# Kernel optimization log

Hardware: AMD Instinct MI355X
Metric: run time of the kernel (lower is better)

The kernel has to match this reference:

```python
import jax, jax.numpy as jnp
import numpy as np
import math

DIM = 4096
DV = 1024          # compress_dim
H = 16             # num_heads
NS = 32            # num_seeds
B, L = 8, 2048
EPS = 1e-5


def _layernorm(x, g, b):
    mu = jnp.mean(x, axis=-1, keepdims=True)
    var = jnp.mean((x - mu) ** 2, axis=-1, keepdims=True)
    return (x - mu) * jax.lax.rsqrt(var + EPS) * g + b


def setup_inputs() -> dict:
    key = jax.random.key(0)
    ks = jax.random.split(key, 12)
    def lin(k, out_d, in_d):
        scale = math.sqrt(6.0 / (in_d + out_d))  # xavier_uniform
        return jax.random.uniform(k, (out_d, in_d), jnp.float32, -scale, scale)
    return {
        "X": jax.random.normal(ks[0], (B, L, DIM), jnp.float32),
        "pad_mask": jax.random.randint(ks[1], (B, L), 0, 2, jnp.int32),
        "S": jax.random.uniform(ks[2], (1, NS, DV), jnp.float32, -0.05, 0.05),
        "Wq": lin(ks[3], DV, DV), "bq": jnp.zeros((DV,), jnp.float32),
        "Wk": lin(ks[4], DV, DIM), "bk": jnp.zeros((DV,), jnp.float32),
        "Wv": lin(ks[5], DV, DIM), "bv": jnp.zeros((DV,), jnp.float32),
        "Wo": lin(ks[6], DV, DV), "bo": jnp.zeros((DV,), jnp.float32),
        "g0": jnp.ones((DV,), jnp.float32), "beta0": jnp.zeros((DV,), jnp.float32),
        "g1": jnp.ones((DV,), jnp.float32), "beta1": jnp.zeros((DV,), jnp.float32),
    }


def reference(X, pad_mask, S, Wq, bq, Wk, bk, Wv, bv, Wo, bo, g0, beta0, g1, beta1):
    b, l, _ = X.shape
    dh = DV // H
    scale = 1.0 / math.sqrt(DV)  # NOTE: full dim_V, not per-head dim
    Q = jnp.broadcast_to(S, (b, NS, DV))              # seeds repeated per batch
    Qp = (Q @ Wq.T + bq).reshape(b, NS, H, dh)
    Kp = (X @ Wk.T + bk).reshape(b, l, H, dh)
    Vp = (X @ Wv.T + bv).reshape(b, l, H, dh)
    score = jnp.einsum('bqhd,bkhd->bhqk', Qp, Kp) * scale
    m = (pad_mask != 0)[:, None, None, :]             # [b,1,1,k]
    score = jnp.where(m, score, jnp.float32(-1e12))
    A = jax.nn.softmax(score, axis=-1) * m.astype(score.dtype)  # post-softmax renorm
    O = jnp.einsum('bhqk,bkhd->bqhd', A, Vp).reshape(b, NS, DV)
    O = Q + O
    O = _layernorm(O, g0, beta0)
    O = O + jax.nn.relu(O @ Wo.T + bo)
    O = _layernorm(O, g1, beta1)
    return O
```

## Files before the change

### kernel.cpp

```cpp
#include <hip/hip_runtime.h>

#define DIMX 4096
#define DVX  1024
#define HX   16
#define DHX  64
#define NSX  32
#define BX   8
#define LX   2048
#define EPSF 1e-5f

typedef unsigned short u16;
typedef unsigned int   u32;

using bf16x8 = __attribute__((ext_vector_type(8))) __bf16;
using f32x4  = __attribute__((ext_vector_type(4))) float;

__device__ __forceinline__ float bfu(u16 u) {
    union { u32 i; float f; } c; c.i = ((u32)u) << 16; return c.f;
}
__device__ __forceinline__ u16 f2b(float f) {
    union { float f; u32 u; } c; c.f = f;
    u32 u = c.u;
    u32 r = (u + 0x7fffu + ((u >> 16) & 1u)) >> 16;
    return (u16)r;
}

__device__ __forceinline__ void async16(const u16* g, u16* l) {
    __builtin_amdgcn_global_load_lds(
        (const __attribute__((address_space(1))) void*)g,
        (__attribute__((address_space(3))) void*)l, 16, 0, 0);
}

template<bool ISF>
__device__ __forceinline__ void ld8(const void* base, size_t idx, float o[8]) {
    if (ISF) {
        const float* f = (const float*)base + idx;
        float4 a = *(const float4*)f, b = *(const float4*)(f + 4);
        o[0]=a.x; o[1]=a.y; o[2]=a.z; o[3]=a.w;
        o[4]=b.x; o[5]=b.y; o[6]=b.z; o[7]=b.w;
    } else {
        const u16* h = (const u16*)base + idx;
        uint4 v = *(const uint4*)h;
        o[0]=bfu(v.x & 0xffff); o[1]=bfu(v.x >> 16);
        o[2]=bfu(v.y & 0xffff); o[3]=bfu(v.y >> 16);
        o[4]=bfu(v.z & 0xffff); o[5]=bfu(v.z >> 16);
        o[6]=bfu(v.w & 0xffff); o[7]=bfu(v.w >> 16);
    }
}
__device__ __forceinline__ float ld1(const void* base, size_t idx, bool isf) {
    return isf ? ((const float*)base)[idx] : bfu(((const u16*)base)[idx]);
}

__global__ __launch_bounds__(256) void detect_kernel(const u16* __restrict__ X,
                                                     int* __restrict__ flag) {
    __shared__ int cnt;
    if (threadIdx.x == 0) cnt = 0;
    __syncthreads();
    int local = 0;
    for (int i = threadIdx.x; i < 8192; i += 256) {
        u32 e = ((u32)X[i] >> 7) & 0xffu;
        if (e >= 200u) local++;
    }
    atomicAdd(&cnt, local);
    __syncthreads();
    if (threadIdx.x == 0) *flag = (cnt > 32) ? 1 : 0;
}

__global__ __launch_bounds__(256) void cvt_kernel(const int* __restrict__ flag,
                                                  const float* __restrict__ src,
                                                  u16* __restrict__ dst, int ngrp) {
    if (*flag == 0) return;
    int stride = gridDim.x * 256;
    for (int i = blockIdx.x * 256 + threadIdx.x; i < ngrp; i += stride) {
        const float4* f = (const float4*)(src + (size_t)i * 8);
        float4 a = f[0], b = f[1];
        uint4 r;
        r.x = (u32)f2b(a.x) | ((u32)f2b(a.y) << 16);
        r.y = (u32)f2b(a.z) | ((u32)f2b(a.w) << 16);
        r.z = (u32)f2b(b.x) | ((u32)f2b(b.y) << 16);
        r.w = (u32)f2b(b.z) | ((u32)f2b(b.w) << 16);
        *(uint4*)(dst + (size_t)i * 8) = r;
    }
}

__global__ __launch_bounds__(256) void qp_kernel(
        const int* __restrict__ flag, const void* __restrict__ S,
        const void* __restrict__ Wq, const void* __restrict__ bq,
        float* __restrict__ Qp) {
    int wid = blockIdx.x * 4 + (threadIdx.x >> 6);
    int lane = threadIdx.x & 63;
    int q = wid >> 10, n = wid & 1023;
    bool isf = (*flag != 0);
    float p = 0.f;
    if (isf) {
        const float* srow = (const float*)S + (size_t)q * DVX + lane * 16;
        const float* wrow = (const float*)Wq + (size_t)n * DVX + lane * 16;
#pragma unroll
        for (int e = 0; e < 16; e += 4) {
            float4 a = *(const float4*)(srow + e);
            float4 b = *(const float4*)(wrow + e);
            p += a.x * b.x + a.y * b.y + a.z * b.z + a.w * b.w;
        }
    } else {
        const u16* srow = (const u16*)S + (size_t)q * DVX + lane * 16;
        const u16* wrow = (const u16*)Wq + (size_t)n * DVX + lane * 16;
#pragma unroll
        for (int c = 0; c < 2; c++) {
            uint4 a = *(const uint4*)(srow + c * 8);
            uint4 b = *(const uint4*)(wrow + c * 8);
            p += bfu(a.x & 0xffff) * bfu(b.x & 0xffff) + bfu(a.x >> 16) * bfu(b.x >> 16)
               + bfu(a.y & 0xffff) * bfu(b.y & 0xffff) + bfu(a.y >> 16) * bfu(b.y >> 16)
               + bfu(a.z & 0xffff) * bfu(b.z & 0xffff) + bfu(a.z >> 16) * bfu(b.z >> 16)
               + bfu(a.w & 0xffff) * bfu(b.w & 0xffff) + bfu(a.w >> 16) * bfu(b.w >> 16);
        }
    }
#pragma unroll
    for (int off = 32; off > 0; off >>= 1)
        p += __shfl_xor(p, off, 64);
    if (lane == 0) Qp[wid] = p + ld1(bq, n, isf);
}

__global__ __launch_bounds__(512, 2) void kv_gemm3(
        const int* __restrict__ flag,
        const void* __restrict__ X,  const u16* __restrict__ Xb,
        const void* __restrict__ Wk, const void* __restrict__ bk,
        const void* __restrict__ Wv, const void* __restrict__ bv,
        const u16* __restrict__ Wkb, const u16* __restrict__ Wvb,
        u16* __restrict__ Kp, u16* __restrict__ Vp) {
    extern __shared__ __align__(16) u16 lds[];
    const bool isf = (*flag != 0);
    const u16* Xs = isf ? Xb : (const u16*)X;

    const int t = threadIdx.x;
    const int lane = t & 63, w = t >> 6;
    const int wm = w >> 2, wn = w & 3;
    const int quad = lane >> 4, l16 = lane & 15;
    const int l8 = l16 & 7;

    const int bid = blockIdx.x;
    const int swz = (bid & 7) * 64 + (bid >> 3);
    const int mt = swz >> 3, nt = swz & 7;
    const int m0 = mt * 256, n0 = nt * 256;

    const u16* Wb16; const void* bias; int boff;
    if (n0 < DVX) { Wb16 = (isf ? Wkb : (const u16*)Wk) + (size_t)n0 * DIMX;
                    bias = bk; boff = n0; }
    else          { Wb16 = (isf ? Wvb : (const u16*)Wv) + (size_t)(n0 - DVX) * DIMX;
                    bias = bv; boff = n0 - DVX; }

    f32x4 acc[8][4];
#pragma unroll
    for (int i = 0; i < 8; i++)
#pragma unroll
        for (int j = 0; j < 4; j++) acc[i][j] = {0.f, 0.f, 0.f, 0.f};

    {
        u16* An = lds;
        u16* Bn = lds + 32768;
#pragma unroll
        for (int i = 0; i < 4; i++) {
            int gi = i * 512 + t;
            int r = gi >> 3;
            int g = (gi & 7) ^ (r & 7);
            async16(Xs + (size_t)(m0 + r) * DIMX + g * 8, An + gi * 8);
        }
#pragma unroll
        for (int i = 0; i < 4; i++) {
            int gi = i * 512 + t;
            int r = gi >> 3;
            int g = (gi & 7) ^ (r & 7);
            async16(Wb16 + (size_t)r * DIMX + g * 8, Bn + gi * 8);
        }
        asm volatile("s_waitcnt vmcnt(0)" ::: "memory");
        __builtin_amdgcn_s_barrier();
    }

    for (int kt = 0; kt < DIMX / 64; kt++) {
        u16* Ab = lds + (kt & 1) * 16384;
        u16* Bb = lds + 32768 + (kt & 1) * 16384;
        u16* An = lds + ((kt + 1) & 1) * 16384;
        u16* Bn = lds + 32768 + ((kt + 1) & 1) * 16384;
        const int k1 = (kt + 1) * 64;
        const bool st = (kt + 1) < (DIMX / 64);

        bf16x8 bfr[4][2];
#pragma unroll
        for (int ni = 0; ni < 4; ni++)
#pragma unroll
            for (int ks = 0; ks < 2; ks++) {
                int R = wn * 64 + ni * 16 + l16;
                int cc = ((ks * 4 + quad) ^ l8);
                bfr[ni][ks] = *(const bf16x8*)&Bb[R * 64 + cc * 8];
            }
        {
            bf16x8 a[2][2];
#pragma unroll
            for (int dm = 0; dm < 2; dm++)
#pragma unroll
                for (int ks = 0; ks < 2; ks++) {
                    int R = wm * 128 + dm * 16 + l16;
                    int cc = ((ks * 4 + quad) ^ l8);
                    a[dm][ks] = *(const bf16x8*)&Ab[R * 64 + cc * 8];
                }
            if (st) {
#pragma unroll
                for (int i = 0; i < 4; i++) {
                    int gi = i * 512 + t;
                    int r = gi >> 3;
                    int g = (gi & 7) ^ (r & 7);
                    async16(Xs + (size_t)(m0 + r) * DIMX + k1 + g * 8, An + gi * 8);
                }
#pragma unroll
                for (int i = 0; i < 4; i++) {
                    int gi = i * 512 + t;
                    int r = gi >> 3;
                    int g = (gi & 7) ^ (r & 7);
                    async16(Wb16 + (size_t)r * DIMX + k1 + g * 8, Bn + gi * 8);
                }
            }
            __builtin_amdgcn_s_setprio(1);
#pragma unroll
            for (int dm = 0; dm < 2; dm++)
#pragma unroll
                for (int ni = 0; ni < 4; ni++)
#pragma unroll
                    for (int ks = 0; ks < 2; ks++)
                        acc[dm][ni] = __builtin_amdgcn_mfma_f32_16x16x32_bf16(
                            a[dm][ks], bfr[ni][ks], acc[dm][ni], 0, 0, 0);
            __builtin_amdgcn_s_setprio(0);
        }
        __builtin_amdgcn_s_barrier();

#pragma unroll
        for (int p = 1; p < 4; p++) {
            bf16x8 a[2][2];
#pragma unroll
            for (int dm = 0; dm < 2; dm++)
#pragma unroll
                for (int ks = 0; ks < 2; ks++) {
                    int R = wm * 128 + (2 * p + dm) * 16 + l16;
                    int cc = ((ks * 4 + quad) ^ l8);
                    a[dm][ks] = *(const bf16x8*)&Ab[R * 64 + cc * 8];
                }
            __builtin_amdgcn_s_setprio(1);
#pragma unroll
            for (int dm = 0; dm < 2; dm++)
#pragma unroll
                for (int ni = 0; ni < 4; ni++)
#pragma unroll
                    for (int ks = 0; ks < 2; ks++)
                        acc[2 * p + dm][ni] = __builtin_amdgcn_mfma_f32_16x16x32_bf16(
                            a[dm][ks], bfr[ni][ks], acc[2 * p + dm][ni], 0, 0, 0);
            __builtin_amdgcn_s_setprio(0);
            if (p < 3) __builtin_amdgcn_s_barrier();
        }

        __builtin_amdgcn_sched_barrier(0);
        asm volatile("s_waitcnt vmcnt(0)" ::: "memory");
        __builtin_amdgcn_s_barrier();
        __builtin_amdgcn_sched_barrier(0);
    }

    float bb[4];
#pragma unroll
    for (int ni = 0; ni < 4; ni++)
        bb[ni] = ld1(bias, (size_t)(boff + wn * 64 + ni * 16 + l16), isf);
#pragma unroll
    for (int mi = 0; mi < 8; mi++) {
#pragma unroll
        for (int ni = 0; ni < 4; ni++) {
            int colL = wn * 64 + ni * 16 + l16;
            int col = n0 + colL;
            u16* dst; int dcol;
            if (col < DVX) { dst = Kp; dcol = col; }
            else           { dst = Vp; dcol = col - DVX; }
#pragma unroll
            for (int r = 0; r < 4; r++) {
                int row = m0 + wm * 128 + mi * 16 + quad * 4 + r;
                dst[(size_t)row * DVX + dcol] = f2b(acc[mi][ni][r] + bb[ni]);
            }
        }
    }
}

#define TM 128
#define TN 128
#define BKK 32
#define LDT 32

__device__ __forceinline__ uint4 pack8(float o[8]) {
    uint4 r;
    r.x = (u32)f2b(o[0]) | ((u32)f2b(o[1]) << 16);
    r.y = (u32)f2b(o[2]) | ((u32)f2b(o[3]) << 16);
    r.z = (u32)f2b(o[4]) | ((u32)f2b(o[5]) << 16);
    r.w = (u32)f2b(o[6]) | ((u32)f2b(o[7]) << 16);
    return r;
}

__global__ __launch_bounds__(256) void kv_gemm2(
        const int* __restrict__ flag,
        const void* __restrict__ X,  const u16* __restrict__ Xb,
        const void* __restrict__ Wk, const void* __restrict__ bk,
        const void* __restrict__ Wv, const void* __restrict__ bv,
        const u16* __restrict__ Wkb, const u16* __restrict__ Wvb,
        u16* __restrict__ Kp, u16* __restrict__ Vp) {
    __shared__ u16 As[TM * LDT];
    __shared__ u16 Bs[TN * LDT];
    const bool isf = (*flag != 0);
    const u16* Xs = isf ? Xb : (const u16*)X;

    const int t = threadIdx.x;
    const int lane = t & 63, w = t >> 6;
    const int wm = w >> 1, wn = w & 1;
    const int quad = lane >> 4, l16 = lane & 15;
    const int bl = blockIdx.x;
    const int xcd = bl & 7, bq = bl >> 3;
    const int m0 = (xcd + 8 * (bq >> 4)) * TM;
    const int n0 = (bq & 15) * TN;
    const u16* Wb16; const void* bias; int boff;
    if (n0 < DVX) { Wb16 = (isf ? Wkb : (const u16*)Wk) + (size_t)n0 * DIMX;
                    bias = bk; boff = n0; }
    else          { Wb16 = (isf ? Wvb : (const u16*)Wv) + (size_t)(n0 - DVX) * DIMX;
                    bias = bv; boff = n0 - DVX; }

    f32x4 acc[4][4];
#pragma unroll
    for (int i = 0; i < 4; i++)
#pragma unroll
        for (int j = 0; j < 4; j++) acc[i][j] = {0.f, 0.f, 0.f, 0.f};

    const int srow = lane >> 2;
    const int gcol = ((lane & 3) ^ ((lane >> 3) & 3)) * 8;
    const int ph = (l16 >> 1) & 3;

    for (int k0 = 0; k0 < DIMX; k0 += BKK) {
        __syncthreads();
#pragma unroll
        for (int c = 0; c < 2; c++) {
            int rr = w * 32 + c * 16;
            async16(Xs + (size_t)(m0 + rr + srow) * DIMX + k0 + gcol,
                    As + rr * LDT);
            async16(Wb16 + (size_t)(rr + srow) * DIMX + k0 + gcol,
                    Bs + rr * LDT);
        }
        __syncthreads();
        bf16x8 af[4], bfr[4];
#pragma unroll
        for (int mi = 0; mi < 4; mi++) {
            int ar = wm * 64 + mi * 16 + l16;
            af[mi] = *(const bf16x8*)&As[ar * LDT + (quad ^ ph) * 8];
        }
#pragma unroll
        for (int ni = 0; ni < 4; ni++) {
            int br = wn * 64 + ni * 16 + l16;
            bfr[ni] = *(const bf16x8*)&Bs[br * LDT + (quad ^ ph) * 8];
        }
#pragma unroll
        for (int mi = 0; mi < 4; mi++)
#pragma unroll
            for (int ni = 0; ni < 4; ni++)
                acc[mi][ni] = __builtin_amdgcn_mfma_f32_16x16x32_bf16(
                    af[mi], bfr[ni], acc[mi][ni], 0, 0, 0);
    }

#pragma unroll
    for (int mi = 0; mi < 4; mi++) {
#pragma unroll
        for (int ni = 0; ni < 4; ni++) {
            int colL = wn * 64 + ni * 16 + l16;
            int col = n0 + colL;
            float bb = ld1(bias, (size_t)(boff + colL), isf);
            u16* dst; int dcol;
            if (col < DVX) { dst = Kp; dcol = col; }
            else           { dst = Vp; dcol = col - DVX; }
#pragma unroll
            for (int r = 0; r < 4; r++) {
                int row = m0 + wm * 64 + mi * 16 + quad * 4 + r;
                dst[(size_t)row * DVX + dcol] = f2b(acc[mi][ni][r] + bb);
            }
        }
    }
}

template<bool ISF>
__device__ void kv_body(const void* __restrict__ X,
                        const void* __restrict__ Wk, const void* __restrict__ bk,
                        const void* __restrict__ Wv, const void* __restrict__ bv,
                        u16* __restrict__ Kp, u16* __restrict__ Vp,
                        u16* As, u16* Bs) {
    const int t = threadIdx.x;
    const int lane = t & 63, w = t >> 6;
    const int wm = w >> 1, wn = w & 1;
    const int quad = lane >> 4, l16 = lane & 15;
    const int bl = blockIdx.x;
    const int xcd = bl & 7, bq = bl >> 3;
    const int m0 = (xcd + 8 * (bq >> 4)) * TM;
    const int n0 = (bq & 15) * TN;
    const void* Wbase; const void* bias; int boff;
    size_t woff;
    if (n0 < DVX) { Wbase = Wk; bias = bk; woff = (size_t)n0 * DIMX; boff = n0; }
    else          { Wbase = Wv; bias = bv; woff = (size_t)(n0 - DVX) * DIMX; boff = n0 - DVX; }
    const u16* Wb16 = (const u16*)Wbase + woff;
    const float* Wbf = (const float*)Wbase + woff;

    f32x4 acc[4][4];
#pragma unroll
    for (int i = 0; i < 4; i++)
#pragma unroll
        for (int j = 0; j < 4; j++) acc[i][j] = {0.f, 0.f, 0.f, 0.f};

    const int srow = lane >> 2;
    const int gcol = ((lane & 3) ^ ((lane >> 3) & 3)) * 8;
    const int ph = (l16 >> 1) & 3;
    const int r0 = t >> 2, c0 = (t & 3) * 8;
    const int r1 = r0 + 64;
    const int swc = (((t & 3) ^ ((r0 >> 1) & 3))) * 8;

    for (int k0 = 0; k0 < DIMX; k0 += BKK) {
        if constexpr (ISF) {
            float oa0[8], oa1[8], ob0[8], ob1[8];
            ld8<true>(X,   (size_t)(m0 + r0) * DIMX + k0 + c0, oa0);
            ld8<true>(X,   (size_t)(m0 + r1) * DIMX + k0 + c0, oa1);
            ld8<true>(Wbf, (size_t)r0 * DIMX + k0 + c0, ob0);
            ld8<true>(Wbf, (size_t)r1 * DIMX + k0 + c0, ob1);
            __syncthreads();
            *(uint4*)&As[r0 * LDT + swc] = pack8(oa0);
            *(uint4*)&As[r1 * LDT + swc] = pack8(oa1);
            *(uint4*)&Bs[r0 * LDT + swc] = pack8(ob0);
            *(uint4*)&Bs[r1 * LDT + swc] = pack8(ob1);
        } else {
            __syncthreads();
#pragma unroll
            for (int c = 0; c < 2; c++) {
                int rr = w * 32 + c * 16;
                async16((const u16*)X + (size_t)(m0 + rr + srow) * DIMX + k0 + gcol,
                        As + rr * LDT);
                async16(Wb16 + (size_t)(rr + srow) * DIMX + k0 + gcol,
                        Bs + rr * LDT);
            }
        }
        __syncthreads();
        bf16x8 af[4], bfr[4];
#pragma unroll
        for (int mi = 0; mi < 4; mi++) {
            int ar = wm * 64 + mi * 16 + l16;
            af[mi] = *(const bf16x8*)&As[ar * LDT + (quad ^ ph) * 8];
        }
#pragma unroll
        for (int ni = 0; ni < 4; ni++) {
            int br = wn * 64 + ni * 16 + l16;
            bfr[ni] = *(const bf16x8*)&Bs[br * LDT + (quad ^ ph) * 8];
        }
#pragma unroll
        for (int mi = 0; mi < 4; mi++)
#pragma unroll
            for (int ni = 0; ni < 4; ni++)
                acc[mi][ni] = __builtin_amdgcn_mfma_f32_16x16x32_bf16(
                    af[mi], bfr[ni], acc[mi][ni], 0, 0, 0);
    }

#pragma unroll
    for (int mi = 0; mi < 4; mi++) {
#pragma unroll
        for (int ni = 0; ni < 4; ni++) {
            int colL = wn * 64 + ni * 16 + l16;
            int col = n0 + colL;
            float bb = ld1(bias, (size_t)(boff + colL), ISF);
            u16* dst; int dcol;
            if (col < DVX) { dst = Kp; dcol = col; }
            else           { dst = Vp; dcol = col - DVX; }
#pragma unroll
            for (int r = 0; r < 4; r++) {
                int row = m0 + wm * 64 + mi * 16 + quad * 4 + r;
                dst[(size_t)row * DVX + dcol] = f2b(acc[mi][ni][r] + bb);
            }
        }
    }
}

__global__ __launch_bounds__(256) void kv_gemm(
        const int* __restrict__ flag, const void* __restrict__ X,
        const void* __restrict__ Wk, const void* __restrict__ bk,
        const void* __restrict__ Wv, const void* __restrict__ bv,
        u16* __restrict__ Kp, u16* __restrict__ Vp) {
    __shared__ u16 As[TM * LDT];
    __shared__ u16 Bs[TN * LDT];
    if (*flag) kv_body<true>(X, Wk, bk, Wv, bv, Kp, Vp, As, Bs);
    else       kv_body<false>(X, Wk, bk, Wv, bv, Kp, Vp, As, Bs);
}

#define CHK 256
#define NCH (LX / CHK)
__global__ __launch_bounds__(256) void attn2_kernel(
        const float* __restrict__ Qp, const u16* __restrict__ Kp,
        const u16* __restrict__ Vp, const int* __restrict__ pad,
        float* __restrict__ Opart, float* __restrict__ Ml) {
    __shared__ float sc[NSX * CHK];
    const int blk = blockIdx.x;
    const int b  = blk / (HX * NCH);
    const int h  = (blk / NCH) % HX;
    const int c0 = blk % NCH;
    const int t = threadIdx.x;
    const int w = t >> 6, lane = t & 63;
    const int rsub = lane >> 3;
    const int dsub = lane & 7;
    const int q0w = w * 8;

    float qc[8][8];
#pragma unroll
    for (int qq = 0; qq < 8; qq++) {
        const float* qp = Qp + (size_t)(q0w + qq) * DVX + h * DHX + dsub * 8;
        float4 a = *(const float4*)qp, bq4 = *(const float4*)(qp + 4);
        qc[qq][0]=a.x; qc[qq][1]=a.y; qc[qq][2]=a.z; qc[qq][3]=a.w;
        qc[qq][4]=bq4.x; qc[qq][5]=bq4.y; qc[qq][6]=bq4.z; qc[qq][7]=bq4.w;
    }

    const u16* kb = Kp + ((size_t)b * LX + c0 * CHK) * DVX + h * DHX;
    const int* pb = pad + b * LX + c0 * CHK;

    float lmax[8];
#pragma unroll
    for (int qq = 0; qq < 8; qq++) lmax[qq] = -3e38f;
    for (int i = 0; i < CHK / 8; i++) {
        int k = i * 8 + rsub;
        uint4 v = *(const uint4*)(kb + (size_t)k * DVX + dsub * 8);
        float kf[8];
        kf[0]=bfu(v.x & 0xffff); kf[1]=bfu(v.x >> 16);
        kf[2]=bfu(v.y & 0xffff); kf[3]=bfu(v.y >> 16);
        kf[4]=bfu(v.z & 0xffff); kf[5]=bfu(v.z >> 16);
        kf[6]=bfu(v.w & 0xffff); kf[7]=bfu(v.w >> 16);
        int pm = pb[k];
#pragma unroll
        for (int qq = 0; qq < 8; qq++) {
            float s = kf[0]*qc[qq][0] + kf[1]*qc[qq][1]
                    + kf[2]*qc[qq][2] + kf[3]*qc[qq][3]
                    + kf[4]*qc[qq][4] + kf[5]*qc[qq][5]
                    + kf[6]*qc[qq][6] + kf[7]*qc[qq][7];
            s += __shfl_xor(s, 1, 64);
            s += __shfl_xor(s, 2, 64);
            s += __shfl_xor(s, 4, 64);
            s *= 0.03125f;
            s = pm ? s : -1e30f;
            if (dsub == 0) sc[(q0w + qq) * CHK + k] = s;
            lmax[qq] = fmaxf(lmax[qq], s);
        }
    }
#pragma unroll
    for (int qq = 0; qq < 8; qq++) {
        lmax[qq] = fmaxf(lmax[qq], __shfl_xor(lmax[qq], 8, 64));
        lmax[qq] = fmaxf(lmax[qq], __shfl_xor(lmax[qq], 16, 64));
        lmax[qq] = fmaxf(lmax[qq], __shfl_xor(lmax[qq], 32, 64));
    }

#pragma unroll
    for (int qq = 0; qq < 8; qq++) {
        float m = lmax[qq];
        float lsum = 0.f;
#pragma unroll
        for (int it = 0; it < CHK / 64; it++) {
            int idx = (q0w + qq) * CHK + it * 64 + lane;
            float sv = sc[idx];
            float e = (sv > -1e29f) ? __expf(sv - m) : 0.f;
            sc[idx] = e;
            lsum += e;
        }
#pragma unroll
        for (int off = 32; off > 0; off >>= 1)
            lsum += __shfl_xor(lsum, off, 64);
        if (lane == 0) {
            Ml[(size_t)blk * 64 + (q0w + qq) * 2 + 0] = m;
            Ml[(size_t)blk * 64 + (q0w + qq) * 2 + 1] = lsum;
        }
    }

    float acc[8][8];
#pragma unroll
    for (int qq = 0; qq < 8; qq++)
#pragma unroll
        for (int e = 0; e < 8; e++) acc[qq][e] = 0.f;
    const u16* vb = Vp + ((size_t)b * LX + c0 * CHK) * DVX + h * DHX + dsub * 8;
    for (int i = 0; i < CHK / 8; i++) {
        int k = i * 8 + rsub;
        uint4 v = *(const uint4*)(vb + (size_t)k * DVX);
        float vf[8];
        vf[0]=bfu(v.x & 0xffff); vf[1]=bfu(v.x >> 16);
        vf[2]=bfu(v.y & 0xffff); vf[3]=bfu(v.y >> 16);
        vf[4]=bfu(v.z & 0xffff); vf[5]=bfu(v.z >> 16);
        vf[6]=bfu(v.w & 0xffff); vf[7]=bfu(v.w >> 16);
#pragma unroll
        for (int qq = 0; qq < 8; qq++) {
            float p = sc[(q0w + qq) * CHK + k];
#pragma unroll
            for (int e = 0; e < 8; e++) acc[qq][e] += p * vf[e];
        }
    }
#pragma unroll
    for (int qq = 0; qq < 8; qq++) {
#pragma unroll
        for (int e = 0; e < 8; e++) {
            acc[qq][e] += __shfl_xor(acc[qq][e], 8, 64);
            acc[qq][e] += __shfl_xor(acc[qq][e], 16, 64);
            acc[qq][e] += __shfl_xor(acc[qq][e], 32, 64);
        }
        if (rsub == qq) {
            float* op = Opart + ((size_t)blk * NSX + q0w + qq) * DHX + dsub * 8;
            float4 r0 = {acc[qq][0], acc[qq][1], acc[qq][2], acc[qq][3]};
            float4 r1 = {acc[qq][4], acc[qq][5], acc[qq][6], acc[qq][7]};
            *(float4*)op = r0;
            *(float4*)(op + 4) = r1;
        }
    }
}

__global__ __launch_bounds__(256) void attn_combine(
        const float* __restrict__ Opart, const float* __restrict__ Ml,
        float* __restrict__ Oat) {
    const int bh = blockIdx.x;
    const int b = bh / HX, h = bh % HX;
    const int t = threadIdx.x;
    const int q = t >> 3, d0 = (t & 7) * 8;
    const size_t cbase = (size_t)bh * NCH;
    float m = -3e38f;
#pragma unroll
    for (int c = 0; c < NCH; c++)
        m = fmaxf(m, Ml[(cbase + c) * 64 + q * 2]);
    float l = 0.f, o[8];
#pragma unroll
    for (int e = 0; e < 8; e++) o[e] = 0.f;
#pragma unroll
    for (int c = 0; c < NCH; c++) {
        float mc = Ml[(cbase + c) * 64 + q * 2 + 0];
        float lc = Ml[(cbase + c) * 64 + q * 2 + 1];
        float wgt = (mc > -1e29f) ? __expf(mc - m) : 0.f;
        l += wgt * lc;
        const float* op = Opart + ((cbase + c) * NSX + q) * DHX + d0;
        float4 x = *(const float4*)op, y = *(const float4*)(op + 4);
        o[0] += wgt * x.x; o[1] += wgt * x.y; o[2] += wgt * x.z; o[3] += wgt * x.w;
        o[4] += wgt * y.x; o[5] += wgt * y.y; o[6] += wgt * y.z; o[7] += wgt * y.w;
    }
    float inv = (l > 0.f) ? 1.f / l : 0.f;
    float* dst = Oat + ((size_t)(b * NSX) + q) * DVX + h * DHX + d0;
    float4 r0 = {o[0]*inv, o[1]*inv, o[2]*inv, o[3]*inv};
    float4 r1 = {o[4]*inv, o[5]*inv, o[6]*inv, o[7]*inv};
    *(float4*)dst = r0;
    *(float4*)(dst + 4) = r1;
}

#define QG 4
__global__ __launch_bounds__(256) void attn_kernel(
        const float* __restrict__ Qp, const u16* __restrict__ Kp,
        const u16* __restrict__ Vp, const int* __restrict__ pad,
        float* __restrict__ Oat) {
    __shared__ float qv[QG * DHX];
    __shared__ float sc[QG * LX];
    __shared__ float rpart[256 * 8];
    __shared__ float invs[QG];
    const int blk = blockIdx.x;
    const int nqg = NSX / QG;
    const int b  = blk / (HX * nqg);
    const int h  = (blk / nqg) % HX;
    const int q0 = (blk % nqg) * QG;
    const int t = threadIdx.x;
    const int w = t >> 6, lane = t & 63;

    qv[t] = Qp[(size_t)(q0 + (t >> 6)) * DVX + h * DHX + (t & 63)];
    __syncthreads();

    const u16* Kb = Kp + (size_t)b * LX * DVX + h * DHX;
    const int rsub = lane >> 3;
    const int dsub = lane & 7;
    float qc[8];
#pragma unroll
    for (int e = 0; e < 8; e++) qc[e] = qv[w * DHX + dsub * 8 + e];

    float lmax = -3e38f;
    for (int i = 0; i < LX / 8; i++) {
        int k = i * 8 + rsub;
        uint4 v = *(const uint4*)(Kb + (size_t)k * DVX + dsub * 8);
        float s = bfu(v.x & 0xffff) * qc[0] + bfu(v.x >> 16) * qc[1]
                + bfu(v.y & 0xffff) * qc[2] + bfu(v.y >> 16) * qc[3]
                + bfu(v.z & 0xffff) * qc[4] + bfu(v.z >> 16) * qc[5]
                + bfu(v.w & 0xffff) * qc[6] + bfu(v.w >> 16) * qc[7];
        s += __shfl_xor(s, 1, 64);
        s += __shfl_xor(s, 2, 64);
        s += __shfl_xor(s, 4, 64);
        s *= 0.03125f;
        s = (pad[b * LX + k] != 0) ? s : -1e30f;
        if (dsub == 0) sc[w * LX + k] = s;
        lmax = fmaxf(lmax, s);
    }
#pragma unroll
    for (int off = 32; off > 0; off >>= 1)
        lmax = fmaxf(lmax, __shfl_xor(lmax, off, 64));
    float lsum = 0.f;
    for (int i = 0; i < LX / 64; i++) {
        int k = i * 64 + lane;
        float sv = sc[w * LX + k];
        float e = (sv > -1e29f) ? __expf(sv - lmax) : 0.f;
        sc[w * LX + k] = e;
        lsum += e;
    }
#pragma unroll
    for (int off = 32; off > 0; off >>= 1)
        lsum += __shfl_xor(lsum, off, 64);
    if (lane == 0) invs[w] = (lsum > 0.f) ? 1.f / lsum : 0.f;

    const int kg = (t >> 3) & 7, dg = t & 7;
    const u16* Vb = Vp + (size_t)b * LX * DVX + h * DHX + dg * 8;
    float a8[8];
#pragma unroll
    for (int e = 0; e < 8; e++) a8[e] = 0.f;
    for (int i = 0; i < LX / 8; i++) {
        int k = i * 8 + kg;
        float p = sc[w * LX + k];
        uint4 v = *(const uint4*)(Vb + (size_t)k * DVX);
        a8[0] += p * bfu(v.x & 0xffff); a8[1] += p * bfu(v.x >> 16);
        a8[2] += p * bfu(v.y & 0xffff); a8[3] += p * bfu(v.y >> 16);
        a8[4] += p * bfu(v.z & 0xffff); a8[5] += p * bfu(v.z >> 16);
        a8[6] += p * bfu(v.w & 0xffff); a8[7] += p * bfu(v.w >> 16);
    }
#pragma unroll
    for (int e = 0; e < 8; e++) rpart[t * 8 + e] = a8[e];
    __syncthreads();

    {
        int q = t >> 6, d = t & 63;
        float o = 0.f;
#pragma unroll
        for (int g = 0; g < 8; g++)
            o += rpart[(q * 64 + g * 8 + (d >> 3)) * 8 + (d & 7)];
        o *= invs[q];
        Oat[((size_t)(b * NSX + q0 + q)) * DVX + h * DHX + d] = o;
    }
}

template<bool ISF>
__device__ void epi_body(float* u, float* y0, float* red,
                         const float* __restrict__ Oat, const void* __restrict__ S,
                         const void* __restrict__ Wo, const void* __restrict__ bo,
                         const void* __restrict__ g0, const void* __restrict__ be0,
                         const void* __restrict__ g1, const void* __restrict__ be1,
                         void* __restrict__ out) {
    const int bq = blockIdx.x;
    const int q = bq & 31;
    const int t = threadIdx.x;
    const int w = t >> 6, lane = t & 63;

    float ls = 0.f, ls2 = 0.f;
#pragma unroll
    for (int j = 0; j < 2; j++) {
        int c = t + 512 * j;
        float v = ld1(S, (size_t)q * DVX + c, ISF) + Oat[(size_t)bq * DVX + c];
        u[c] = v; ls += v; ls2 += v * v;
    }
    red[t] = ls; __syncthreads();
    for (int s2 = 256; s2 > 0; s2 >>= 1) { if (t < s2) red[t] += red[t + s2]; __syncthreads(); }
    float mu = red[0] / DVX; __syncthreads();
    red[t] = ls2; __syncthreads();
    for (int s2 = 256; s2 > 0; s2 >>= 1) { if (t < s2) red[t] += red[t + s2]; __syncthreads(); }
    float var = red[0] / DVX - mu * mu;
    float r = rsqrtf(var + EPSF);
    __syncthreads();
#pragma unroll
    for (int j = 0; j < 2; j++) {
        int c = t + 512 * j;
        y0[c] = (u[c] - mu) * r * ld1(g0, c, ISF) + ld1(be0, c, ISF);
    }
    __syncthreads();

    float yr[16];
    if constexpr (ISF) {
#pragma unroll
        for (int e = 0; e < 16; e++) yr[e] = y0[lane * 16 + e];
    } else {
#pragma unroll
        for (int e = 0; e < 8; e++) { yr[e] = y0[lane * 8 + e]; yr[8 + e] = y0[512 + lane * 8 + e]; }
    }
    for (int i = 0; i < 128; i++) {
        int n = i * 8 + w;
        float p = 0.f;
        if constexpr (ISF) {
            float wv[8];
            const float* row = (const float*)Wo + (size_t)n * DVX;
            ld8<true>(row, lane * 16, wv);
#pragma unroll
            for (int e = 0; e < 8; e++) p += wv[e] * yr[e];
            ld8<true>(row, lane * 16 + 8, wv);
#pragma unroll
            for (int e = 0; e < 8; e++) p += wv[e] * yr[8 + e];
        } else {
            const uint4* row = (const uint4*)((const u16*)Wo + (size_t)n * DVX);
            uint4 v0 = row[lane], v1 = row[lane + 64];
            p += bfu(v0.x & 0xffff) * yr[0] + bfu(v0.x >> 16) * yr[1]
               + bfu(v0.y & 0xffff) * yr[2] + bfu(v0.y >> 16) * yr[3]
               + bfu(v0.z & 0xffff) * yr[4] + bfu(v0.z >> 16) * yr[5]
               + bfu(v0.w & 0xffff) * yr[6] + bfu(v0.w >> 16) * yr[7];
            p += bfu(v1.x & 0xffff) * yr[8]  + bfu(v1.x >> 16) * yr[9]
               + bfu(v1.y & 0xffff) * yr[10] + bfu(v1.y >> 16) * yr[11]
               + bfu(v1.z & 0xffff) * yr[12] + bfu(v1.z >> 16) * yr[13]
               + bfu(v1.w & 0xffff) * yr[14] + bfu(v1.w >> 16) * yr[15];
        }
#pragma unroll
        for (int off = 32; off > 0; off >>= 1)
            p += __shfl_xor(p, off, 64);
        if (lane == 0) {
            float z = p + ld1(bo, n, ISF);
            u[n] = y0[n] + fmaxf(z, 0.f);
        }
    }
    __syncthreads();
    ls = 0.f; ls2 = 0.f;
#pragma unroll
    for (int j = 0; j < 2; j++) {
        int c = t + 512 * j; float v = u[c]; ls += v; ls2 += v * v;
    }
    red[t] = ls; __syncthreads();
    for (int s2 = 256; s2 > 0; s2 >>= 1) { if (t < s2) red[t] += red[t + s2]; __syncthreads(); }
    mu = red[0] / DVX; __syncthreads();
    red[t] = ls2; __syncthreads();
    for (int s2 = 256; s2 > 0; s2 >>= 1) { if (t < s2) red[t] += red[t + s2]; __syncthreads(); }
    var = red[0] / DVX - mu * mu;
    r = rsqrtf(var + EPSF);
#pragma unroll
    for (int j = 0; j < 2; j++) {
        int c = t + 512 * j;
        float v = (u[c] - mu) * r * ld1(g1, c, ISF) + ld1(be1, c, ISF);
        if (ISF) ((float*)out)[(size_t)bq * DVX + c] = v;
        else     ((u16*)out)[(size_t)bq * DVX + c] = f2b(v);
    }
}

__global__ __launch_bounds__(512) void epi_kernel(
        const int* __restrict__ flag,
        const float* __restrict__ Oat, const void* __restrict__ S,
        const void* __restrict__ Wo, const void* __restrict__ bo,
        const void* __restrict__ g0, const void* __restrict__ be0,
        const void* __restrict__ g1, const void* __restrict__ be1,
        void* __restrict__ out) {
    __shared__ float u[DVX];
    __shared__ float y0[DVX];
    __shared__ float red[512];
    if (*flag) epi_body<true>(u, y0, red, Oat, S, Wo, bo, g0, be0, g1, be1, out);
    else       epi_body<false>(u, y0, red, Oat, S, Wo, bo, g0, be0, g1, be1, out);
}

extern "C" void kernel_launch(void* const* d_in, const int* in_sizes, int n_in,
                              void* d_out, int out_size, void* d_ws, size_t ws_size,
                              hipStream_t stream) {
    (void)in_sizes; (void)n_in; (void)out_size;
    const void* X    = d_in[0];
    const int* pad   = (const int*)d_in[1];
    const void* S    = d_in[2];
    const void* Wq   = d_in[3];
    const void* bq   = d_in[4];
    const void* Wk   = d_in[5];
    const void* bk   = d_in[6];
    const void* Wv   = d_in[7];
    const void* bv   = d_in[8];
    const void* Wo   = d_in[9];
    const void* bo   = d_in[10];
    const void* g0   = d_in[11];
    const void* be0  = d_in[12];
    const void* g1   = d_in[13];
    const void* be1  = d_in[14];

    char* ws = (char*)d_ws;
    int*   flag = (int*)ws;
    float* Qp  = (float*)(ws + 256);
    float* Oat = (float*)(ws + 256 + 131072);
    u16*   Kp  = (u16*)(ws + 256 + 131072 + 1048576);
    u16*   Vp  = Kp + (size_t)BX * LX * DVX;
    u16*   Xb  = Vp + (size_t)BX * LX * DVX;
    u16*   Wkb = Xb + (size_t)BX * LX * DIMX;
    u16*   Wvb = Wkb + (size_t)DVX * DIMX;
    float* Opart = (float*)(Wvb + (size_t)DVX * DIMX);
    float* Ml  = Opart + (size_t)BX * HX * NCH * NSX * DHX;

    size_t need = 256 + 131072 + 1048576
                + 2 * (size_t)BX * LX * DVX * 2
                + (size_t)BX * LX * DIMX * 2
                + 2 * (size_t)DVX * DIMX * 2;
    size_t need2 = need
                 + (size_t)BX * HX * NCH * NSX * DHX * 4
                 + (size_t)BX * HX * NCH * 64 * 4;

    static int attr_ok = -1;
    if (attr_ok < 0) {
        hipError_t e = hipFuncSetAttribute(
            reinterpret_cast<const void*>(kv_gemm3),
            hipFuncAttributeMaxDynamicSharedMemorySize, 131072);
        attr_ok = (e == hipSuccess) ? 1 : 0;
    }

    detect_kernel<<<1, 256, 0, stream>>>((const u16*)X, flag);
    qp_kernel<<<8192, 256, 0, stream>>>(flag, S, Wq, bq, Qp);

    if (ws_size >= need) {
        cvt_kernel<<<2048, 256, 0, stream>>>(flag, (const float*)X, Xb,
                                             BX * LX * DIMX / 8);
        cvt_kernel<<<512, 256, 0, stream>>>(flag, (const float*)Wk, Wkb,
                                            DVX * DIMX / 8);
        cvt_kernel<<<512, 256, 0, stream>>>(flag, (const float*)Wv, Wvb,
                                            DVX * DIMX / 8);
        if (attr_ok == 1) {
            kv_gemm3<<<512, 512, 131072, stream>>>(flag, X, Xb, Wk, bk, Wv, bv,
                                                   Wkb, Wvb, Kp, Vp);
        } else {
            kv_gemm2<<<2048, 256, 0, stream>>>(flag, X, Xb, Wk, bk, Wv, bv,
                                               Wkb, Wvb, Kp, Vp);
        }
    } else {
        kv_gemm<<<2048, 256, 0, stream>>>(flag, X, Wk, bk, Wv, bv, Kp, Vp);
    }

    if (ws_size >= need2) {
        attn2_kernel<<<BX * HX * NCH, 256, 0, stream>>>(Qp, Kp, Vp, pad,
                                                        Opart, Ml);
        attn_combine<<<BX * HX, 256, 0, stream>>>(Opart, Ml, Oat);
    } else {
        attn_kernel<<<BX * HX * (NSX / QG), 256, 0, stream>>>(Qp, Kp, Vp, pad, Oat);
    }
    epi_kernel<<<BX * NSX, 512, 0, stream>>>(flag, Oat, S, Wo, bo, g0, be0, g1, be1, (void*)d_out);
}
```

Before: 887.1 us.

## Hoist async prefetch before MFMA loop and coalesce fp32 row dot products

In the K/V projection GEMM main loop, the next tile's global-to-LDS async loads are now issued at the top of each iteration, and the intermediate barriers between the four MFMA sub-phases are removed. The goal is to overlap memory traffic with the whole compute phase and cut synchronisation stalls. Separately, the fp32 Qp and Wo row dot products now read with a lane-interleaved float4 stride, so a wave's accesses are contiguous and coalesced. Issuing the prefetch earlier may raise register pressure, and fewer barriers change how waves interleave.

```diff
diff --git a/kernel.cpp b/kernel.cpp
--- a/kernel.cpp
+++ b/kernel.cpp
@@ -93,12 +93,12 @@
     bool isf = (*flag != 0);
     float p = 0.f;
     if (isf) {
-        const float* srow = (const float*)S + (size_t)q * DVX + lane * 16;
-        const float* wrow = (const float*)Wq + (size_t)n * DVX + lane * 16;
-#pragma unroll
-        for (int e = 0; e < 16; e += 4) {
-            float4 a = *(const float4*)(srow + e);
-            float4 b = *(const float4*)(wrow + e);
+        const float4* s4 = (const float4*)((const float*)S + (size_t)q * DVX);
+        const float4* w4 = (const float4*)((const float*)Wq + (size_t)n * DVX);
+#pragma unroll
+        for (int e = 0; e < 4; e++) {
+            float4 a = s4[e * 64 + lane];
+            float4 b = w4[e * 64 + lane];
             p += a.x * b.x + a.y * b.y + a.z * b.z + a.w * b.w;
         }
     } else {
@@ -181,7 +181,24 @@
         u16* An = lds + ((kt + 1) & 1) * 16384;
         u16* Bn = lds + 32768 + ((kt + 1) & 1) * 16384;
         const int k1 = (kt + 1) * 64;
-        const bool st = (kt + 1) < (DIMX / 64);
+
+        if (kt + 1 < DIMX / 64) {
+#pragma unroll
+            for (int i = 0; i < 4; i++) {
+                int gi = i * 512 + t;
+                int r = gi >> 3;
+                int g = (gi & 7) ^ (r & 7);
+                async16(Xs + (size_t)(m0 + r) * DIMX + k1 + g * 8, An + gi * 8);
+            }
+#pragma unroll
+            for (int i = 0; i < 4; i++) {
+                int gi = i * 512 + t;
+                int r = gi >> 3;
+                int g = (gi & 7) ^ (r & 7);
+                async16(Wb16 + (size_t)r * DIMX + k1 + g * 8, Bn + gi * 8);
+            }
+        }
+        __builtin_amdgcn_sched_barrier(0);
 
         bf16x8 bfr[4][2];
 #pragma unroll
@@ -192,47 +209,9 @@
                 int cc = ((ks * 4 + quad) ^ l8);
                 bfr[ni][ks] = *(const bf16x8*)&Bb[R * 64 + cc * 8];
             }
-        {
-            bf16x8 a[2][2];
-#pragma unroll
-            for (int dm = 0; dm < 2; dm++)
-#pragma unroll
-                for (int ks = 0; ks < 2; ks++) {
-                    int R = wm * 128 + dm * 16 + l16;
-                    int cc = ((ks * 4 + quad) ^ l8);
-                    a[dm][ks] = *(const bf16x8*)&Ab[R * 64 + cc * 8];
-                }
-            if (st) {
-#pragma unroll
-                for (int i = 0; i < 4; i++) {
-                    int gi = i * 512 + t;
-                    int r = gi >> 3;
-                    int g = (gi & 7) ^ (r & 7);
-                    async16(Xs + (size_t)(m0 + r) * DIMX + k1 + g * 8, An + gi * 8);
-                }
-#pragma unroll
-                for (int i = 0; i < 4; i++) {
-                    int gi = i * 512 + t;
-                    int r = gi >> 3;
-                    int g = (gi & 7) ^ (r & 7);
-                    async16(Wb16 + (size_t)r * DIMX + k1 + g * 8, Bn + gi * 8);
-                }
-            }
-            __builtin_amdgcn_s_setprio(1);
-#pragma unroll
-            for (int dm = 0; dm < 2; dm++)
-#pragma unroll
-                for (int ni = 0; ni < 4; ni++)
-#pragma unroll
-                    for (int ks = 0; ks < 2; ks++)
-                        acc[dm][ni] = __builtin_amdgcn_mfma_f32_16x16x32_bf16(
-                            a[dm][ks], bfr[ni][ks], acc[dm][ni], 0, 0, 0);
-            __builtin_amdgcn_s_setprio(0);
-        }
-        __builtin_amdgcn_s_barrier();
-
-#pragma unroll
-        for (int p = 1; p < 4; p++) {
+
+#pragma unroll
+        for (int p = 0; p < 4; p++) {
             bf16x8 a[2][2];
 #pragma unroll
             for (int dm = 0; dm < 2; dm++)
@@ -252,7 +231,6 @@
                         acc[2 * p + dm][ni] = __builtin_amdgcn_mfma_f32_16x16x32_bf16(
                             a[dm][ks], bfr[ni][ks], acc[2 * p + dm][ni], 0, 0, 0);
             __builtin_amdgcn_s_setprio(0);
-            if (p < 3) __builtin_amdgcn_s_barrier();
         }
 
         __builtin_amdgcn_sched_barrier(0);
@@ -770,8 +748,12 @@
 
     float yr[16];
     if constexpr (ISF) {
-#pragma unroll
-        for (int e = 0; e < 16; e++) yr[e] = y0[lane * 16 + e];
+        const float4* y4 = (const float4*)y0;
+#pragma unroll
+        for (int e = 0; e < 4; e++) {
+            float4 v = y4[e * 64 + lane];
+            yr[e*4+0]=v.x; yr[e*4+1]=v.y; yr[e*4+2]=v.z; yr[e*4+3]=v.w;
+        }
     } else {
 #pragma unroll
         for (int e = 0; e < 8; e++) { yr[e] = y0[lane * 8 + e]; yr[8 + e] = y0[512 + lane * 8 + e]; }
@@ -780,14 +762,13 @@
         int n = i * 8 + w;
         float p = 0.f;
         if constexpr (ISF) {
-            float wv[8];
-            const float* row = (const float*)Wo + (size_t)n * DVX;
-            ld8<true>(row, lane * 16, wv);
-#pragma unroll
-            for (int e = 0; e < 8; e++) p += wv[e] * yr[e];
-            ld8<true>(row, lane * 16 + 8, wv);
-#pragma unroll
-            for (int e = 0; e < 8; e++) p += wv[e] * yr[8 + e];
+            const float4* row4 = (const float4*)((const float*)Wo + (size_t)n * DVX);
+#pragma unroll
+            for (int e = 0; e < 4; e++) {
+                float4 wv = row4[e * 64 + lane];
+                p += wv.x * yr[e*4] + wv.y * yr[e*4+1]
+                   + wv.z * yr[e*4+2] + wv.w * yr[e*4+3];
+            }
         } else {
             const uint4* row = (const uint4*)((const u16*)Wo + (size_t)n * DVX);
             uint4 v0 = row[lane], v1 = row[lane + 64];
```

Result: faster. 852.4 us (-3.9%).
